# Optimization experiments

Hardware: AMD Instinct MI355X
Metric: run time of the kernel (lower is better)

The kernel has to match this reference:

```python
import jax, jax.numpy as jnp
import numpy as np

B, S, D = 2, 2048, 2048
H, KVH, HD = 8, 1, 256          # query heads, kv heads, head_dim (GQA: n_rep = H // KVH)
ROPE_THETA = 10000.0
NEG_INF = -1e9


def setup_inputs() -> dict:
    key = jax.random.key(0)
    k1, k2, k3, k4, k5 = jax.random.split(key, 5)
    hidden_states = jax.random.normal(k1, (B, S, D), dtype=jnp.float32)
    # additive causal mask: 0 where allowed, -inf where masked, shape (B,1,S,S)
    causal = jnp.tril(jnp.ones((S, S), dtype=bool))
    attention_mask = jnp.where(causal, 0.0, NEG_INF).astype(jnp.float32)
    attention_mask = jnp.broadcast_to(attention_mask[None, None], (B, 1, S, S))
    position_ids = jnp.broadcast_to(jnp.arange(S, dtype=jnp.int32)[None, :], (B, S))
    sc = 0.02
    Wq = jax.random.normal(k2, (H * HD, D), dtype=jnp.float32) * sc   # torch Linear weight layout [out,in]
    Wk = jax.random.normal(k3, (KVH * HD, D), dtype=jnp.float32) * sc
    Wv = jax.random.normal(k4, (KVH * HD, D), dtype=jnp.float32) * sc
    Wo = jax.random.normal(k5, (D, H * HD), dtype=jnp.float32) * sc
    return {"hidden_states": hidden_states, "attention_mask": attention_mask,
            "position_ids": position_ids, "Wq": Wq, "Wk": Wk, "Wv": Wv, "Wo": Wo}


def _rotate_half(x):
    x1, x2 = jnp.split(x, 2, axis=-1)
    return jnp.concatenate((-x2, x1), axis=-1)


def _rope_cos_sin(position_ids):
    inv_freq = 1.0 / (ROPE_THETA ** (jnp.arange(0, HD, 2, dtype=jnp.float32) / HD))  # [HD/2]
    freqs = position_ids.astype(jnp.float32)[:, :, None] * inv_freq[None, None, :]   # [B,S,HD/2]
    emb = jnp.concatenate((freqs, freqs), axis=-1)                                   # [B,S,HD]
    return jnp.cos(emb)[:, None], jnp.sin(emb)[:, None]                              # [B,1,S,HD]


def reference(hidden_states, attention_mask, position_ids, Wq, Wk, Wv, Wo):
    q = (hidden_states @ Wq.T).reshape(B, S, H, HD).transpose(0, 2, 1, 3)     # [B,H,S,HD]
    k = (hidden_states @ Wk.T).reshape(B, S, KVH, HD).transpose(0, 2, 1, 3)   # [B,KVH,S,HD]
    v = (hidden_states @ Wv.T).reshape(B, S, KVH, HD).transpose(0, 2, 1, 3)
    cos, sin = _rope_cos_sin(position_ids)
    q = q * cos + _rotate_half(q) * sin
    k = k * cos + _rotate_half(k) * sin
    n_rep = H // KVH
    k = jnp.repeat(k, n_rep, axis=1)                                          # repeat_kv -> [B,H,S,HD]
    v = jnp.repeat(v, n_rep, axis=1)
    scores = jnp.einsum('bhqd,bhkd->bhqk', q, k) / jnp.sqrt(jnp.float32(HD))
    scores = scores + attention_mask
    attn = jax.nn.softmax(scores, axis=-1)                                    # dropout p=0 (eval)
    ctx = jnp.einsum('bhqk,bhkd->bhqd', attn, v)
    ctx = ctx.transpose(0, 2, 1, 3).reshape(B, S, H * HD)
    out = ctx @ Wo.T
    return out, attn
```

## Files before the change

kernel.cpp:

```cpp
#include <hip/hip_runtime.h>
#include <hip/hip_bf16.h>
#include <math.h>

typedef __bf16 bf16_t;
typedef __bf16 bf16x8 __attribute__((ext_vector_type(8)));
typedef float  f32x4  __attribute__((ext_vector_type(4)));

#define DEV __device__ __forceinline__

constexpr int B_   = 2;
constexpr int S_   = 2048;
constexpr int D_   = 2048;
constexpr int H_   = 8;
constexpr int HD_  = 256;
constexpr int NQKV_ = H_ * HD_ + 2 * HD_;
constexpr int TOK_ = B_ * S_;

#if defined(__has_builtin)
#if __has_builtin(__builtin_amdgcn_global_load_lds)
#define HAS_GLLDS 1
#endif
#endif

DEV void stage16(const bf16_t* g, bf16_t* l) {
#ifdef HAS_GLLDS
  __builtin_amdgcn_global_load_lds((const __attribute__((address_space(1))) void*)g,
                                   (__attribute__((address_space(3))) void*)l, 16, 0, 0);
#else
  *(bf16x8*)l = *(const bf16x8*)g;
#endif
}

__global__ void cast_inputs(const float* __restrict__ hs, const float* __restrict__ wq,
                            const float* __restrict__ wk, const float* __restrict__ wv,
                            const float* __restrict__ wo,
                            bf16_t* __restrict__ Xb, bf16_t* __restrict__ Wqkvb,
                            bf16_t* __restrict__ Wob) {
  const size_t i = (size_t)blockIdx.x * blockDim.x + threadIdx.x;
  const size_t NHS = (size_t)TOK_ * D_;
  const size_t NWQ = (size_t)H_ * HD_ * D_;
  const size_t NWK = (size_t)HD_ * D_;
  if (i < NHS) Xb[i] = (bf16_t)hs[i];
  if (i < NWQ) { Wqkvb[i] = (bf16_t)wq[i]; Wob[i] = (bf16_t)wo[i]; }
  if (i < NWK) { Wqkvb[NWQ + i] = (bf16_t)wk[i]; Wqkvb[NWQ + NWK + i] = (bf16_t)wv[i]; }
}

template <bool CBF16>
__global__ __launch_bounds__(256, 2)
void gemm_bt(const bf16_t* __restrict__ Ab, const bf16_t* __restrict__ Bg,
             void* __restrict__ Cv, int K, int lda, int ldb, int ldc)
{
  const int bn = blockIdx.x, bm = blockIdx.y;
  const int m0 = bm * 128, n0 = bn * 128;

  __shared__ __align__(16) bf16_t Asm[128 * 32];
  __shared__ __align__(16) bf16_t Bsm[128 * 32];

  const int tid  = threadIdx.x;
  const int l    = tid & 63;
  const int w    = tid >> 6;
  const int wm   = (w >> 1) * 64;
  const int wn   = (w & 1) * 64;
  const int lrow = l & 15;
  const int quad = l >> 4;

  f32x4 acc[4][4] = {};

  for (int k0 = 0; k0 < K; k0 += 32) {
    __syncthreads();
    #pragma unroll
    for (int c = 0; c < 2; ++c) {
      int chunk = c * 256 + tid;
      int row = chunk >> 2, col = (chunk & 3) << 3;
      stage16(Ab + (size_t)(m0 + row) * lda + (k0 + col), &Asm[row * 32 + col]);
      stage16(Bg + (size_t)(n0 + row) * ldb + (k0 + col), &Bsm[row * 32 + col]);
    }
    __syncthreads();

    bf16x8 af[4], bfr[4];
    #pragma unroll
    for (int i = 0; i < 4; ++i)
      af[i] = *(const bf16x8*)&Asm[(wm + i * 16 + lrow) * 32 + quad * 8];
    #pragma unroll
    for (int j = 0; j < 4; ++j)
      bfr[j] = *(const bf16x8*)&Bsm[(wn + j * 16 + lrow) * 32 + quad * 8];
    #pragma unroll
    for (int i = 0; i < 4; ++i)
      #pragma unroll
      for (int j = 0; j < 4; ++j)
        acc[i][j] = __builtin_amdgcn_mfma_f32_16x16x32_bf16(af[i], bfr[j], acc[i][j], 0, 0, 0);
  }

  #pragma unroll
  for (int i = 0; i < 4; ++i) {
    int row = wm + i * 16 + quad * 4;
    #pragma unroll
    for (int j = 0; j < 4; ++j) {
      int col = n0 + wn + j * 16 + lrow;
      #pragma unroll
      for (int r = 0; r < 4; ++r) {
        if (CBF16) ((bf16_t*)Cv)[(size_t)(m0 + row + r) * ldc + col] = (bf16_t)acc[i][j][r];
        else       ((float*) Cv)[(size_t)(m0 + row + r) * ldc + col] = acc[i][j][r];
      }
    }
  }
}

__global__ void rope_kernel(const bf16_t* __restrict__ qkv, const int* __restrict__ pos_ids,
                            bf16_t* __restrict__ Qh, bf16_t* __restrict__ Kb,
                            bf16_t* __restrict__ Vt)
{
  const int t = blockIdx.x;
  const int b = t >> 11, s = t & (S_ - 1);
  const int tid = threadIdx.x;
  const int pd = tid & 127, half = tid >> 7;
  const float pos = (float)pos_ids[t];
  const float expo = (float)(2 * pd) * (1.0f / 256.0f);
  const float invf = 1.0f / powf(10000.0f, expo);
  const float ang = pos * invf;
  const float c = cosf(ang), sn = sinf(ang);
  const bf16_t* base = qkv + (size_t)t * NQKV_;
  const int other = half ? tid - 128 : tid + 128;
  const float sgn = half ? 1.0f : -1.0f;
  #pragma unroll
  for (int h = 0; h < H_; ++h) {
    float x = (float)base[h * HD_ + tid];
    float xo = (float)base[h * HD_ + other];
    Qh[((size_t)(b * H_ + h) * S_ + s) * HD_ + tid] = (bf16_t)(x * c + sgn * xo * sn);
  }
  {
    float x = (float)base[D_ + tid], xo = (float)base[D_ + other];
    Kb[(size_t)t * HD_ + tid] = (bf16_t)(x * c + sgn * xo * sn);
  }
  Vt[((size_t)b * HD_ + tid) * S_ + s] = base[D_ + HD_ + tid];
}

constexpr int PSTR = 136;

DEV void compute_S(const bf16_t* __restrict__ Kg, bf16_t* __restrict__ KV,
                   const bf16x8 aq[8], f32x4 accS[8],
                   int kb, int tid, int lrow, int quad)
{
  #pragma unroll
  for (int half = 0; half < 2; ++half) {
    __syncthreads();
    #pragma unroll
    for (int it = 0; it < 8; ++it) {
      int s = it * 256 + tid;
      int c = s >> 6, key = s & 63;
      stage16(Kg + (size_t)(kb * 128 + half * 64 + key) * HD_ + c * 8, KV + s * 8);
    }
    __syncthreads();
    #pragma unroll
    for (int kk = 0; kk < 8; ++kk) {
      bf16x8 bk[4];
      #pragma unroll
      for (int j = 0; j < 4; ++j)
        bk[j] = *(const bf16x8*)&KV[((kk * 4 + quad) * 64 + j * 16 + lrow) * 8];
      #pragma unroll
      for (int j = 0; j < 4; ++j)
        accS[half * 4 + j] =
            __builtin_amdgcn_mfma_f32_16x16x32_bf16(aq[kk], bk[j], accS[half * 4 + j], 0, 0, 0);
    }
  }
}

__global__ __launch_bounds__(256, 2)
void flash_attn(const bf16_t* __restrict__ Qh, const bf16_t* __restrict__ Kbp,
                const bf16_t* __restrict__ Vt, float* __restrict__ attn,
                bf16_t* __restrict__ Ctx)
{
  const int z = blockIdx.x;
  const int qb = blockIdx.y;
  const int b = z >> 3, h = z & 7;
  const int q0 = qb * 64;
  const bf16_t* Qg = Qh + ((size_t)z * S_ + q0) * HD_;
  const bf16_t* Kg = Kbp + (size_t)b * S_ * HD_;
  const bf16_t* Vg = Vt + (size_t)b * HD_ * S_;
  float* Pg = attn + (size_t)z * S_ * S_ + (size_t)q0 * S_;

  __shared__ __align__(16) bf16_t KV[64 * 256];
  __shared__ __align__(16) bf16_t Pst[4 * 16 * PSTR];

  const int tid = threadIdx.x;
  const int w = tid >> 6, l = tid & 63;
  const int lrow = l & 15, quad = l >> 4;
  const int nkb = (qb >> 1) + 1;
  const float scale = 0.0625f;

  for (int kb = nkb; kb < S_ / 128; ++kb) {
    #pragma unroll
    for (int it = 0; it < 8; ++it) {
      int idx = it * 256 + tid;
      int row = idx >> 5, c4 = idx & 31;
      *(f32x4*)&Pg[(size_t)row * S_ + kb * 128 + c4 * 4] = f32x4{0.f, 0.f, 0.f, 0.f};
    }
  }

  bf16x8 aq[8];
  const bf16_t* qrow = Qg + (size_t)(w * 16 + lrow) * HD_ + quad * 8;
  #pragma unroll
  for (int kk = 0; kk < 8; ++kk) aq[kk] = *(const bf16x8*)(qrow + kk * 32);

  float m[4], lsum[4];
  #pragma unroll
  for (int r = 0; r < 4; ++r) { m[r] = -3.0e38f; lsum[r] = 0.f; }

  const int rowg0 = q0 + w * 16 + quad * 4;

  for (int kb = 0; kb < nkb; ++kb) {
    f32x4 accS[8] = {};
    compute_S(Kg, KV, aq, accS, kb, tid, lrow, quad);
    #pragma unroll
    for (int r = 0; r < 4; ++r) {
      float sv[8], tmax = -3.0e38f;
      #pragma unroll
      for (int j = 0; j < 8; ++j) {
        float s = accS[j][r] * scale;
        int col = kb * 128 + j * 16 + lrow;
        if (col > rowg0 + r) s = -3.0e38f;
        sv[j] = s;
        tmax = fmaxf(tmax, s);
      }
      #pragma unroll
      for (int o = 1; o < 16; o <<= 1) tmax = fmaxf(tmax, __shfl_xor(tmax, o, 64));
      float mn = fmaxf(m[r], tmax);
      float add = 0.f;
      #pragma unroll
      for (int j = 0; j < 8; ++j) add += __expf(sv[j] - mn);
      #pragma unroll
      for (int o = 1; o < 16; o <<= 1) add += __shfl_xor(add, o, 64);
      lsum[r] = lsum[r] * __expf(m[r] - mn) + add;
      m[r] = mn;
    }
  }

  float mp[4];
  #pragma unroll
  for (int r = 0; r < 4; ++r) mp[r] = m[r] + __logf(lsum[r]);

  f32x4 accO[16] = {};
  bf16_t* pw = &Pst[w * 16 * PSTR];

  for (int kb = 0; kb < nkb; ++kb) {
    f32x4 accS[8] = {};
    compute_S(Kg, KV, aq, accS, kb, tid, lrow, quad);

    #pragma unroll
    for (int r = 0; r < 4; ++r) {
      float* prow = Pg + (size_t)(w * 16 + quad * 4 + r) * S_ + kb * 128;
      #pragma unroll
      for (int j = 0; j < 8; ++j) {
        int col = kb * 128 + j * 16 + lrow;
        float p = (col <= rowg0 + r) ? __expf(accS[j][r] * scale - mp[r]) : 0.f;
        prow[j * 16 + lrow] = p;
        pw[(quad * 4 + r) * PSTR + j * 16 + lrow] = (bf16_t)p;
      }
    }
    bf16x8 ap[4];
    #pragma unroll
    for (int kk2 = 0; kk2 < 4; ++kk2)
      ap[kk2] = *(const bf16x8*)&pw[lrow * PSTR + kk2 * 32 + quad * 8];

    #pragma unroll
    for (int half = 0; half < 2; ++half) {
      __syncthreads();
      #pragma unroll
      for (int it = 0; it < 8; ++it) {
        int s = it * 256 + tid;
        int c2 = s >> 8, d = s & 255;
        stage16(Vg + (size_t)d * S_ + kb * 128 + half * 64 + c2 * 8, KV + s * 8);
      }
      __syncthreads();
      #pragma unroll
      for (int kkl = 0; kkl < 2; ++kkl) {
        #pragma unroll
        for (int j2 = 0; j2 < 16; ++j2) {
          bf16x8 bv = *(const bf16x8*)&KV[((kkl * 4 + quad) * 256 + j2 * 16 + lrow) * 8];
          accO[j2] = __builtin_amdgcn_mfma_f32_16x16x32_bf16(ap[half * 2 + kkl], bv, accO[j2], 0, 0, 0);
        }
      }
    }
  }

  #pragma unroll
  for (int j2 = 0; j2 < 16; ++j2) {
    #pragma unroll
    for (int r = 0; r < 4; ++r) {
      int rowq = q0 + w * 16 + quad * 4 + r;
      Ctx[((size_t)b * S_ + rowq) * D_ + h * HD_ + j2 * 16 + lrow] = (bf16_t)accO[j2][r];
    }
  }
}

extern "C" void kernel_launch(void* const* d_in, const int* in_sizes, int n_in,
                              void* d_out, int out_size, void* d_ws, size_t ws_size,
                              hipStream_t stream)
{
  const float* hs  = (const float*)d_in[0];
  const int*   pos = (const int*)d_in[2];
  const float* wq  = (const float*)d_in[3];
  const float* wk  = (const float*)d_in[4];
  const float* wv  = (const float*)d_in[5];
  const float* wo  = (const float*)d_in[6];

  float* out  = (float*)d_out;
  float* attn = out + (size_t)TOK_ * D_;

  char* ws = (char*)d_ws;
  bf16_t* Xb    = (bf16_t*)(ws);
  bf16_t* Wqkvb = (bf16_t*)(ws + 16777216);
  bf16_t* Wob   = (bf16_t*)(ws + 27262976);
  bf16_t* QKVb  = (bf16_t*)(ws + 35651584);
  bf16_t* Qh    = (bf16_t*)(ws + 56623104);
  bf16_t* Kb    = (bf16_t*)(ws + 73400320);
  bf16_t* Vt    = (bf16_t*)(ws + 75497472);
  bf16_t* Ctx   = (bf16_t*)(ws + 77594624);

  cast_inputs<<<(TOK_ * D_) / 256, 256, 0, stream>>>(hs, wq, wk, wv, wo, Xb, Wqkvb, Wob);
  gemm_bt<true><<<dim3(NQKV_ / 128, TOK_ / 128), 256, 0, stream>>>(
      Xb, Wqkvb, QKVb, D_, D_, D_, NQKV_);
  rope_kernel<<<TOK_, 256, 0, stream>>>(QKVb, pos, Qh, Kb, Vt);
  flash_attn<<<dim3(B_ * H_, S_ / 64), 256, 0, stream>>>(Qh, Kb, Vt, attn, Ctx);
  gemm_bt<false><<<dim3(D_ / 128, TOK_ / 128), 256, 0, stream>>>(
      Ctx, Wob, out, D_, D_, D_, D_);
}
```

Baseline: 667.5 us.

## Drop max-tracking softmax pass and move attention-prob writes to separate kernel

The flash kernel now does a single pass over the keys. It computes unnormalised exp(score) without subtracting a running max, accumulates the row sums, and normalises the context at the end. Writing the full probability matrix moves to a new p_writer kernel that recomputes QK^T per 128x128 tile, writes the normalised probabilities and zero-fills the masked upper tiles. Flash blocks are also remapped so short and long causal rows are paired for load balance. The intent is to remove the second QK pass and the heavy fp32 stores from the attention loop. The cost is a recomputed QK GEMM, and without max subtraction exp can overflow for larger score magnitudes.

```diff
diff --git a/kernel.cpp b/kernel.cpp
--- a/kernel.cpp
+++ b/kernel.cpp
@@ -167,17 +167,18 @@
 
 __global__ __launch_bounds__(256, 2)
 void flash_attn(const bf16_t* __restrict__ Qh, const bf16_t* __restrict__ Kbp,
-                const bf16_t* __restrict__ Vt, float* __restrict__ attn,
-                bf16_t* __restrict__ Ctx)
-{
-  const int z = blockIdx.x;
-  const int qb = blockIdx.y;
+                const bf16_t* __restrict__ Vt, bf16_t* __restrict__ Ctx,
+                float* __restrict__ lsum)
+{
+  const int idx = blockIdx.x;
+  int z, qb;
+  if (idx < 256) { z = idx & 15; qb = idx >> 4; }
+  else           { int j = idx - 256; z = j & 15; qb = 31 - (j >> 4); }
   const int b = z >> 3, h = z & 7;
   const int q0 = qb * 64;
   const bf16_t* Qg = Qh + ((size_t)z * S_ + q0) * HD_;
   const bf16_t* Kg = Kbp + (size_t)b * S_ * HD_;
   const bf16_t* Vg = Vt + (size_t)b * HD_ * S_;
-  float* Pg = attn + (size_t)z * S_ * S_ + (size_t)q0 * S_;
 
   __shared__ __align__(16) bf16_t KV[64 * 256];
   __shared__ __align__(16) bf16_t Pst[4 * 16 * PSTR];
@@ -188,72 +189,27 @@
   const int nkb = (qb >> 1) + 1;
   const float scale = 0.0625f;
 
-  for (int kb = nkb; kb < S_ / 128; ++kb) {
-    #pragma unroll
-    for (int it = 0; it < 8; ++it) {
-      int idx = it * 256 + tid;
-      int row = idx >> 5, c4 = idx & 31;
-      *(f32x4*)&Pg[(size_t)row * S_ + kb * 128 + c4 * 4] = f32x4{0.f, 0.f, 0.f, 0.f};
-    }
-  }
-
   bf16x8 aq[8];
   const bf16_t* qrow = Qg + (size_t)(w * 16 + lrow) * HD_ + quad * 8;
   #pragma unroll
   for (int kk = 0; kk < 8; ++kk) aq[kk] = *(const bf16x8*)(qrow + kk * 32);
 
-  float m[4], lsum[4];
-  #pragma unroll
-  for (int r = 0; r < 4; ++r) { m[r] = -3.0e38f; lsum[r] = 0.f; }
-
   const int rowg0 = q0 + w * 16 + quad * 4;
+  float lp[4] = {0.f, 0.f, 0.f, 0.f};
+  f32x4 accO[16] = {};
+  bf16_t* pw = &Pst[w * 16 * PSTR];
 
   for (int kb = 0; kb < nkb; ++kb) {
     f32x4 accS[8] = {};
     compute_S(Kg, KV, aq, accS, kb, tid, lrow, quad);
+
     #pragma unroll
     for (int r = 0; r < 4; ++r) {
-      float sv[8], tmax = -3.0e38f;
-      #pragma unroll
-      for (int j = 0; j < 8; ++j) {
-        float s = accS[j][r] * scale;
-        int col = kb * 128 + j * 16 + lrow;
-        if (col > rowg0 + r) s = -3.0e38f;
-        sv[j] = s;
-        tmax = fmaxf(tmax, s);
-      }
-      #pragma unroll
-      for (int o = 1; o < 16; o <<= 1) tmax = fmaxf(tmax, __shfl_xor(tmax, o, 64));
-      float mn = fmaxf(m[r], tmax);
-      float add = 0.f;
-      #pragma unroll
-      for (int j = 0; j < 8; ++j) add += __expf(sv[j] - mn);
-      #pragma unroll
-      for (int o = 1; o < 16; o <<= 1) add += __shfl_xor(add, o, 64);
-      lsum[r] = lsum[r] * __expf(m[r] - mn) + add;
-      m[r] = mn;
-    }
-  }
-
-  float mp[4];
-  #pragma unroll
-  for (int r = 0; r < 4; ++r) mp[r] = m[r] + __logf(lsum[r]);
-
-  f32x4 accO[16] = {};
-  bf16_t* pw = &Pst[w * 16 * PSTR];
-
-  for (int kb = 0; kb < nkb; ++kb) {
-    f32x4 accS[8] = {};
-    compute_S(Kg, KV, aq, accS, kb, tid, lrow, quad);
-
-    #pragma unroll
-    for (int r = 0; r < 4; ++r) {
-      float* prow = Pg + (size_t)(w * 16 + quad * 4 + r) * S_ + kb * 128;
       #pragma unroll
       for (int j = 0; j < 8; ++j) {
         int col = kb * 128 + j * 16 + lrow;
-        float p = (col <= rowg0 + r) ? __expf(accS[j][r] * scale - mp[r]) : 0.f;
-        prow[j * 16 + lrow] = p;
+        float p = (col <= rowg0 + r) ? __expf(accS[j][r] * scale) : 0.f;
+        lp[r] += p;
         pw[(quad * 4 + r) * PSTR + j * 16 + lrow] = (bf16_t)p;
       }
     }
@@ -284,11 +240,100 @@
   }
 
   #pragma unroll
+  for (int r = 0; r < 4; ++r) {
+    #pragma unroll
+    for (int o = 1; o < 16; o <<= 1) lp[r] += __shfl_xor(lp[r], o, 64);
+  }
+  float inv[4];
+  #pragma unroll
+  for (int r = 0; r < 4; ++r) inv[r] = 1.0f / lp[r];
+
+  #pragma unroll
   for (int j2 = 0; j2 < 16; ++j2) {
     #pragma unroll
     for (int r = 0; r < 4; ++r) {
       int rowq = q0 + w * 16 + quad * 4 + r;
-      Ctx[((size_t)b * S_ + rowq) * D_ + h * HD_ + j2 * 16 + lrow] = (bf16_t)accO[j2][r];
+      Ctx[((size_t)b * S_ + rowq) * D_ + h * HD_ + j2 * 16 + lrow] = (bf16_t)(accO[j2][r] * inv[r]);
+    }
+  }
+  if (lrow == 0) {
+    #pragma unroll
+    for (int r = 0; r < 4; ++r) lsum[(size_t)z * S_ + rowg0 + r] = lp[r];
+  }
+}
+
+__global__ __launch_bounds__(256, 2)
+void p_writer(const bf16_t* __restrict__ Qh, const bf16_t* __restrict__ Kbp,
+              const float* __restrict__ lsum, float* __restrict__ attn)
+{
+  const int bn = blockIdx.x, bm = blockIdx.y, z = blockIdx.z;
+  const int m0 = bm * 128, n0 = bn * 128;
+  float* Pg = attn + (size_t)z * S_ * S_;
+  const int tid = threadIdx.x;
+
+  if (bn > bm) {
+    #pragma unroll
+    for (int it = 0; it < 16; ++it) {
+      int idx = it * 256 + tid;
+      int row = idx >> 5, c4 = idx & 31;
+      *(f32x4*)&Pg[(size_t)(m0 + row) * S_ + n0 + c4 * 4] = f32x4{0.f, 0.f, 0.f, 0.f};
+    }
+    return;
+  }
+
+  const bf16_t* Ab = Qh + (size_t)z * S_ * HD_;
+  const bf16_t* Bg = Kbp + (size_t)(z >> 3) * S_ * HD_;
+
+  __shared__ __align__(16) bf16_t Asm[128 * 32];
+  __shared__ __align__(16) bf16_t Bsm[128 * 32];
+
+  const int l    = tid & 63;
+  const int w    = tid >> 6;
+  const int wm   = (w >> 1) * 64;
+  const int wn   = (w & 1) * 64;
+  const int lrow = l & 15;
+  const int quad = l >> 4;
+
+  f32x4 acc[4][4] = {};
+
+  for (int k0 = 0; k0 < HD_; k0 += 32) {
+    __syncthreads();
+    #pragma unroll
+    for (int c = 0; c < 2; ++c) {
+      int chunk = c * 256 + tid;
+      int row = chunk >> 2, col = (chunk & 3) << 3;
+      stage16(Ab + (size_t)(m0 + row) * HD_ + (k0 + col), &Asm[row * 32 + col]);
+      stage16(Bg + (size_t)(n0 + row) * HD_ + (k0 + col), &Bsm[row * 32 + col]);
+    }
+    __syncthreads();
+
+    bf16x8 af[4], bfr[4];
+    #pragma unroll
+    for (int i = 0; i < 4; ++i)
+      af[i] = *(const bf16x8*)&Asm[(wm + i * 16 + lrow) * 32 + quad * 8];
+    #pragma unroll
+    for (int j = 0; j < 4; ++j)
+      bfr[j] = *(const bf16x8*)&Bsm[(wn + j * 16 + lrow) * 32 + quad * 8];
+    #pragma unroll
+    for (int i = 0; i < 4; ++i)
+      #pragma unroll
+      for (int j = 0; j < 4; ++j)
+        acc[i][j] = __builtin_amdgcn_mfma_f32_16x16x32_bf16(af[i], bfr[j], acc[i][j], 0, 0, 0);
+  }
+
+  const float scale = 0.0625f;
+  #pragma unroll
+  for (int i = 0; i < 4; ++i) {
+    int row = m0 + wm + i * 16 + quad * 4;
+    #pragma unroll
+    for (int r = 0; r < 4; ++r) {
+      const float il = 1.0f / lsum[(size_t)z * S_ + row + r];
+      float* prow = &Pg[(size_t)(row + r) * S_];
+      #pragma unroll
+      for (int j = 0; j < 4; ++j) {
+        int col = n0 + wn + j * 16 + lrow;
+        prow[col] = (col <= row + r) ? __expf(acc[i][j][r] * scale) * il : 0.f;
+      }
     }
   }
 }
@@ -316,12 +361,14 @@
   bf16_t* Kb    = (bf16_t*)(ws + 73400320);
   bf16_t* Vt    = (bf16_t*)(ws + 75497472);
   bf16_t* Ctx   = (bf16_t*)(ws + 77594624);
+  float*  lsum  = (float* )(ws + 94371840);
 
   cast_inputs<<<(TOK_ * D_) / 256, 256, 0, stream>>>(hs, wq, wk, wv, wo, Xb, Wqkvb, Wob);
   gemm_bt<true><<<dim3(NQKV_ / 128, TOK_ / 128), 256, 0, stream>>>(
       Xb, Wqkvb, QKVb, D_, D_, D_, NQKV_);
   rope_kernel<<<TOK_, 256, 0, stream>>>(QKVb, pos, Qh, Kb, Vt);
-  flash_attn<<<dim3(B_ * H_, S_ / 64), 256, 0, stream>>>(Qh, Kb, Vt, attn, Ctx);
+  flash_attn<<<512, 256, 0, stream>>>(Qh, Kb, Vt, Ctx, lsum);
+  p_writer<<<dim3(S_ / 128, S_ / 128, B_ * H_), 256, 0, stream>>>(Qh, Kb, lsum, attn);
   gemm_bt<false><<<dim3(D_ / 128, TOK_ / 128), 256, 0, stream>>>(
       Ctx, Wob, out, D_, D_, D_, D_);
 }
```

Result: no change. 666.4 us (-0.2%).
